# Kernel optimization log

Hardware: AMD Instinct MI355X
Metric: run time of the kernel (lower is better)

The kernel has to match this reference:

```python
import jax, jax.numpy as jnp
import numpy as np

T, B, V, D, H = 128, 64, 100000, 300, 256


def setup_inputs() -> dict:
    key = jax.random.key(0)
    ks = jax.random.split(key, 11)
    s1 = jax.random.randint(ks[0], (T, B), 0, V)
    s2 = jax.random.randint(ks[1], (T, B), 0, V)
    emb = jax.random.normal(ks[2], (V, D), jnp.float32)
    # PyTorch-style init: ih ~ N(0,0.2)/sqrt(H*D), hh ~ N(0,0.2)/sqrt(H)
    W_ih = jax.random.normal(ks[3], (4 * H, D), jnp.float32) * 0.2 / np.sqrt(H * D)
    W_hh = jax.random.normal(ks[4], (4 * H, H), jnp.float32) * 0.2 / np.sqrt(H)
    b_ih = jax.random.uniform(ks[5], (4 * H,), jnp.float32, -0.5, 0.5)
    b_ih = b_ih.at[H:2 * H].set(2.5)  # forget-gate bias boost as in source
    b_hh = jax.random.uniform(ks[6], (4 * H,), jnp.float32, -0.5, 0.5)
    b_hh = b_hh.at[H:2 * H].set(2.5)
    h0a = jax.random.normal(ks[7], (B, H), jnp.float32) * 0.01
    c0a = jax.random.normal(ks[8], (B, H), jnp.float32) * 0.01
    h0b = jax.random.normal(ks[9], (B, H), jnp.float32) * 0.01
    c0b = jax.random.normal(ks[10], (B, H), jnp.float32) * 0.01
    return {"s1": s1, "s2": s2, "emb": emb, "W_ih": W_ih, "W_hh": W_hh,
            "b_ih": b_ih, "b_hh": b_hh, "h0a": h0a, "c0a": c0a,
            "h0b": h0b, "c0b": c0b}


def _lstm_final_hidden(x, h0, c0, W_ih, W_hh, b_ih, b_hh):
    # x: [T, B, D]. PyTorch gate order: i, f, g, o.
    hdim = h0.shape[-1]
    # Precompute input contribution for all timesteps: [T, B, 4H]
    gx = jnp.einsum('tbd,gd->tbg', x, W_ih) + b_ih + b_hh

    def step(carry, gx_t):
        h, c = carry
        gates = gx_t + h @ W_hh.T  # [B, 4H]
        i = jax.nn.sigmoid(gates[:, 0 * hdim:1 * hdim])
        f = jax.nn.sigmoid(gates[:, 1 * hdim:2 * hdim])
        g = jnp.tanh(gates[:, 2 * hdim:3 * hdim])
        o = jax.nn.sigmoid(gates[:, 3 * hdim:4 * hdim])
        c = f * c + i * g
        h = o * jnp.tanh(c)
        return (h, c), None

    (h, _), _ = jax.lax.scan(step, (h0, c0), gx)
    return h  # [B, H]


def reference(s1, s2, emb, W_ih, W_hh, b_ih, b_hh, h0a, c0a, h0b, c0b):
    xa = emb[s1]  # [T, B, D]
    xb = emb[s2]
    ha = _lstm_final_hidden(xa, h0a, c0a, W_ih, W_hh, b_ih, b_hh)
    hb = _lstm_final_hidden(xb, h0b, c0b, W_ih, W_hh, b_ih, b_hh)
    norm = jnp.sum(jnp.abs(ha - hb), axis=1)  # L1 over hidden dim -> [B]
    y = jnp.clip(jnp.exp(-norm), 1e-7, 1.0 - 1e-7)
    return y.reshape(-1)
```

## Files before the change

kernel.cpp:

```cpp
#include <hip/hip_runtime.h>
#include <hip/hip_fp16.h>
#include <math.h>

#define TSTEPS 128

typedef _Float16 half8 __attribute__((ext_vector_type(8)));
typedef float f32x4 __attribute__((ext_vector_type(4)));
typedef __attribute__((ext_vector_type(2))) _Float16 half2v;

#if __has_builtin(__builtin_amdgcn_fdot2)
#define FDOT2(a, b, c) __builtin_amdgcn_fdot2((a), (b), (c), false)
#else
static __device__ __forceinline__ float FDOT2(half2v a, half2v b, float c) {
    return c + (float)a.x * (float)b.x + (float)a.y * (float)b.y;
}
#endif

static __device__ __forceinline__ half2v h2(unsigned u) {
    union { unsigned x; half2v h; } t; t.x = u; return t.h;
}
static __device__ __forceinline__ unsigned packh2(float lo, float hi) {
    union { unsigned x; half2v h; } t; t.h.x = (_Float16)lo; t.h.y = (_Float16)hi; return t.x;
}
static __device__ __forceinline__ float sigm(float x) { return 1.0f / (1.0f + __expf(-x)); }
static __device__ __forceinline__ float tanh_(float x) { return 1.0f - 2.0f / (1.0f + __expf(2.0f * x)); }

typedef __attribute__((address_space(1))) const unsigned GU;
typedef __attribute__((address_space(3))) unsigned LU;
static __device__ __forceinline__ void glds16(const void* g, void* l) {
    __builtin_amdgcn_global_load_lds((GU*)g, (LU*)(uintptr_t)l, 16, 0, 0);
}

__global__ __launch_bounds__(256) void prep_whh(const float* __restrict__ Whh,
                                                unsigned* __restrict__ W16T) {
    __shared__ float tile[32][259];
    const int blk = blockIdx.x, tid = threadIdx.x;
#pragma unroll
    for (int l = 0; l < 32; ++l) {
        int idx = tid + l * 256;
        int r = idx >> 8, k = idx & 255;
        tile[r][k] = Whh[(size_t)(blk * 32 + r) * 256 + k];
    }
    __syncthreads();
#pragma unroll
    for (int l = 0; l < 16; ++l) {
        int o = tid + l * 256;
        int i = o >> 5, rl = o & 31;
        W16T[(size_t)i * 1024 + blk * 32 + rl] = packh2(tile[rl][2 * i], tile[rl][2 * i + 1]);
    }
}

__global__ __launch_bounds__(256) void gather_x(
    const int* __restrict__ s1, const int* __restrict__ s2,
    const float* __restrict__ emb, _Float16* __restrict__ xf)
{
    const int G = blockIdx.x * 256 + threadIdx.x;
    const int lane = G & 63;
    const int tmp = G >> 6;
    const int ks = tmp % 10;
    const int fr = tmp / 10;
    const int m = fr * 16 + (lane & 15);
    const int tok = (m < 8192) ? s1[m] : s2[m - 8192];
    const float* row = emb + (size_t)tok * 300;
    const int k0 = ks * 32 + ((lane >> 4) & 3) * 4;
    half8 o;
#pragma unroll
    for (int c = 0; c < 2; ++c) {
        const int kc = k0 + c * 16;
#pragma unroll
        for (int j = 0; j < 4; ++j)
            o[c * 4 + j] = (_Float16)((kc + j < 300) ? row[kc + j] : 0.f);
    }
    *(half8*)(xf + (size_t)G * 8) = o;
}

__global__ __launch_bounds__(256) void gather_w(
    const float* __restrict__ Wih, _Float16* __restrict__ wf)
{
    const int G = blockIdx.x * 256 + threadIdx.x;
    const int lane = G & 63;
    const int tmp = G >> 6;
    const int ks = tmp % 10;
    const int fr = tmp / 10;
    const int n = fr * 16 + (lane & 15);
    const float* row = Wih + (size_t)n * 300;
    const int k0 = ks * 32 + ((lane >> 4) & 3) * 4;
    half8 o;
#pragma unroll
    for (int c = 0; c < 2; ++c) {
        const int kc = k0 + c * 16;
#pragma unroll
        for (int j = 0; j < 4; ++j)
            o[c * 4 + j] = (_Float16)((kc + j < 300) ? row[kc + j] : 0.f);
    }
    *(half8*)(wf + (size_t)G * 8) = o;
}

__global__ __launch_bounds__(256) void gx_gemm_mfma(
    const _Float16* __restrict__ xf, const _Float16* __restrict__ wf,
    _Float16* __restrict__ gx16)
{
    __shared__ _Float16 sm[2][8192];
    const int tid = threadIdx.x;
    const int lane = tid & 63, wv = tid >> 6;
    const int wr = wv >> 1, wc = wv & 1;
    const int bm = blockIdx.x & 127, bn = blockIdx.x >> 7;
    const int frM = bm * 8, frN = bn * 8;

    f32x4 acc[4][4] = {};

#define STAGE(buf, ks)                                                              \
    {                                                                               \
        _Pragma("unroll")                                                           \
        for (int i_ = 0; i_ < 2; ++i_) {                                            \
            const int fr_ = wv + 4 * i_;                                            \
            glds16(xf + (((size_t)(frM + fr_) * 10 + (ks)) * 64 + lane) * 8,        \
                   &sm[buf][fr_ * 512 + lane * 8]);                                 \
            glds16(wf + (((size_t)(frN + fr_) * 10 + (ks)) * 64 + lane) * 8,        \
                   &sm[buf][4096 + fr_ * 512 + lane * 8]);                          \
        }                                                                           \
    }

    STAGE(0, 0)
    for (int ks = 0; ks < 10; ++ks) {
        const int cur = ks & 1;
        if (ks < 9) {
            STAGE(cur ^ 1, ks + 1)
            asm volatile("s_waitcnt vmcnt(4)" ::: "memory");
        } else {
            asm volatile("s_waitcnt vmcnt(0)" ::: "memory");
        }
        __syncthreads();
        half8 av[4], bv[4];
#pragma unroll
        for (int i = 0; i < 4; ++i) {
            av[i] = *(const half8*)&sm[cur][(wr * 4 + i) * 512 + lane * 8];
            bv[i] = *(const half8*)&sm[cur][4096 + (wc * 4 + i) * 512 + lane * 8];
        }
#pragma unroll
        for (int i = 0; i < 4; ++i)
#pragma unroll
            for (int j = 0; j < 4; ++j)
                acc[i][j] = __builtin_amdgcn_mfma_f32_16x16x32_f16(av[i], bv[j], acc[i][j], 0, 0, 0);
        __syncthreads();
    }
#undef STAGE

    const int m0 = bm * 128 + wr * 64, n0 = bn * 128 + wc * 64;
    const int rl = ((lane >> 4) & 3) * 4, cl = lane & 15;
#pragma unroll
    for (int i = 0; i < 4; ++i)
#pragma unroll
        for (int j = 0; j < 4; ++j)
#pragma unroll
            for (int r = 0; r < 4; ++r)
                gx16[(size_t)(m0 + i * 16 + rl + r) * 1024 + n0 + j * 16 + cl] =
                    (_Float16)acc[i][j][r];
}

__global__ __launch_bounds__(512) void lstm_rec(
    const unsigned* __restrict__ W16T,
    const unsigned short* __restrict__ gx16,
    const float* __restrict__ bih, const float* __restrict__ bhh,
    const float* __restrict__ h0a, const float* __restrict__ c0a,
    const float* __restrict__ h0b, const float* __restrict__ c0b,
    float* __restrict__ hfin)
{
    extern __shared__ unsigned smem[];
    unsigned* wlds = smem;
    unsigned* hbuf = smem + 512 * 68;
    float*    pre  = (float*)(smem + 512 * 68 + 128);

    const int tid = threadIdx.x;
    const int chain = blockIdx.x;
    const int u = tid & 255, p = tid >> 8;
    const int r0 = (p << 9) + u;
    const int r1 = r0 + 256;

    const float bias0 = bih[r0] + bhh[r0];
    const float bias1 = bih[r1] + bhh[r1];

    unsigned w0[96], w1[96];
#pragma unroll
    for (int i = 0; i < 96; ++i) w0[i] = W16T[(size_t)i * 1024 + r0];
#pragma unroll
    for (int i = 0; i < 96; ++i) w1[i] = W16T[(size_t)i * 1024 + r1];
#pragma unroll
    for (int i = 0; i < 96; ++i) {
        asm volatile("" : "+v"(w0[i]));
        asm volatile("" : "+v"(w1[i]));
    }
    {
        unsigned* mb = wlds + tid * 68;
#pragma unroll
        for (int j = 0; j < 32; ++j) mb[j] = W16T[(size_t)(96 + j) * 1024 + r0];
#pragma unroll
        for (int j = 0; j < 32; ++j) mb[32 + j] = W16T[(size_t)(96 + j) * 1024 + r1];
    }

    float c_state = 0.f;
    if (p == 0) {
        const float* c0 = (chain & 64) ? c0b : c0a;
        const float* h0 = (chain & 64) ? h0b : h0a;
        c_state = c0[(chain & 63) * 256 + u];
        ((_Float16*)hbuf)[u] = (_Float16)h0[(chain & 63) * 256 + u];
    }
    __syncthreads();

    const unsigned short* gxb = gx16 + ((size_t)(chain >> 6) * 8192 + (size_t)(chain & 63)) * 1024;
    const unsigned* mb = wlds + tid * 68;

    for (int t = 0; t < TSTEPS; ++t) {
        const unsigned short gr0 = gxb[(size_t)t * 65536 + r0];
        const unsigned short gr1 = gxb[(size_t)t * 65536 + r1];

        float acc0 = 0.f, acc1 = 0.f;
#pragma unroll
        for (int cc = 0; cc < 24; ++cc) {
            const uint4 hv = *(const uint4*)&hbuf[cc * 4];
            acc0 = FDOT2(h2(w0[cc * 4 + 0]), h2(hv.x), acc0);
            acc1 = FDOT2(h2(w1[cc * 4 + 0]), h2(hv.x), acc1);
            acc0 = FDOT2(h2(w0[cc * 4 + 1]), h2(hv.y), acc0);
            acc1 = FDOT2(h2(w1[cc * 4 + 1]), h2(hv.y), acc1);
            acc0 = FDOT2(h2(w0[cc * 4 + 2]), h2(hv.z), acc0);
            acc1 = FDOT2(h2(w1[cc * 4 + 2]), h2(hv.z), acc1);
            acc0 = FDOT2(h2(w0[cc * 4 + 3]), h2(hv.w), acc0);
            acc1 = FDOT2(h2(w1[cc * 4 + 3]), h2(hv.w), acc1);
        }
#pragma unroll
        for (int cc = 0; cc < 4; ++cc) {
            const uint4 hv0 = *(const uint4*)&hbuf[96 + cc * 8];
            const uint4 hv1 = *(const uint4*)&hbuf[96 + cc * 8 + 4];
            const uint4 wa = *(const uint4*)&mb[cc * 8];
            const uint4 wb = *(const uint4*)&mb[cc * 8 + 4];
            const uint4 wc = *(const uint4*)&mb[32 + cc * 8];
            const uint4 wd = *(const uint4*)&mb[32 + cc * 8 + 4];
            acc0 = FDOT2(h2(wa.x), h2(hv0.x), acc0);  acc1 = FDOT2(h2(wc.x), h2(hv0.x), acc1);
            acc0 = FDOT2(h2(wa.y), h2(hv0.y), acc0);  acc1 = FDOT2(h2(wc.y), h2(hv0.y), acc1);
            acc0 = FDOT2(h2(wa.z), h2(hv0.z), acc0);  acc1 = FDOT2(h2(wc.z), h2(hv0.z), acc1);
            acc0 = FDOT2(h2(wa.w), h2(hv0.w), acc0);  acc1 = FDOT2(h2(wc.w), h2(hv0.w), acc1);
            acc0 = FDOT2(h2(wb.x), h2(hv1.x), acc0);  acc1 = FDOT2(h2(wd.x), h2(hv1.x), acc1);
            acc0 = FDOT2(h2(wb.y), h2(hv1.y), acc0);  acc1 = FDOT2(h2(wd.y), h2(hv1.y), acc1);
            acc0 = FDOT2(h2(wb.z), h2(hv1.z), acc0);  acc1 = FDOT2(h2(wd.z), h2(hv1.z), acc1);
            acc0 = FDOT2(h2(wb.w), h2(hv1.w), acc0);  acc1 = FDOT2(h2(wd.w), h2(hv1.w), acc1);
        }
        acc0 += (float)*(const _Float16*)&gr0 + bias0;
        acc1 += (float)*(const _Float16*)&gr1 + bias1;

        float gi = 0.f, gf = 0.f;
        if (p) {
            pre[u] = tanh_(acc0);
            pre[256 + u] = sigm(acc1);
        } else {
            gi = sigm(acc0);
            gf = sigm(acc1);
        }
        __syncthreads();
        if (!p) {
            c_state = fmaf(gf, c_state, gi * pre[u]);
            const float h = pre[256 + u] * tanh_(c_state);
            ((_Float16*)hbuf)[u] = (_Float16)h;
            if (t == TSTEPS - 1) hfin[(size_t)chain * 256 + u] = h;
        }
        __syncthreads();
    }
}

__global__ __launch_bounds__(256) void final_norm(const float* __restrict__ hfin,
                                                  float* __restrict__ out) {
    __shared__ float ws[4];
    const int b = blockIdx.x, tid = threadIdx.x;
    float d = fabsf(hfin[(size_t)b * 256 + tid] - hfin[(size_t)(64 + b) * 256 + tid]);
#pragma unroll
    for (int off = 32; off; off >>= 1) d += __shfl_down(d, off);
    if ((tid & 63) == 0) ws[tid >> 6] = d;
    __syncthreads();
    if (tid == 0) {
        float n = ws[0] + ws[1] + ws[2] + ws[3];
        float y = expf(-n);
        y = fminf(fmaxf(y, 1e-7f), 1.0f - 1e-7f);
        out[b] = y;
    }
}

extern "C" void kernel_launch(void* const* d_in, const int* in_sizes, int n_in,
                              void* d_out, int out_size, void* d_ws, size_t ws_size,
                              hipStream_t stream) {
    const int*   s1  = (const int*)d_in[0];
    const int*   s2  = (const int*)d_in[1];
    const float* emb = (const float*)d_in[2];
    const float* Wih = (const float*)d_in[3];
    const float* Whh = (const float*)d_in[4];
    const float* bih = (const float*)d_in[5];
    const float* bhh = (const float*)d_in[6];
    const float* h0a = (const float*)d_in[7];
    const float* c0a = (const float*)d_in[8];
    const float* h0b = (const float*)d_in[9];
    const float* c0b = (const float*)d_in[10];
    float* out = (float*)d_out;

    char* ws = (char*)d_ws;
    _Float16* xf   = (_Float16*)ws;
    _Float16* wfp  = (_Float16*)(ws + 10485760);
    _Float16* gx16 = (_Float16*)(ws + (size_t)16 * 1024 * 1024);
    unsigned* W16T = (unsigned*)(ws + 50331648);
    float*    hfin = (float*)(ws + 50855936);

    prep_whh<<<32, 256, 0, stream>>>(Whh, W16T);
    gather_x<<<2560, 256, 0, stream>>>(s1, s2, emb, xf);
    gather_w<<<160, 256, 0, stream>>>(Wih, wfp);
    gx_gemm_mfma<<<1024, 256, 0, stream>>>(xf, wfp, gx16);

    const int rec_lds = (512 * 68 + 128 + 512) * 4;
    lstm_rec<<<128, 512, rec_lds, stream>>>(W16T, (const unsigned short*)gx16,
                                            bih, bhh, h0a, c0a, h0b, c0b, hfin);
    final_norm<<<64, 256, 0, stream>>>(hfin, out);
}
```

Before: 419.0 us.

## Split each LSTM chain across two blocks with flag sync and coalesce embedding gather

```diff
diff --git a/kernel.cpp b/kernel.cpp
--- a/kernel.cpp
+++ b/kernel.cpp
@@ -25,6 +25,11 @@
 static __device__ __forceinline__ float sigm(float x) { return 1.0f / (1.0f + __expf(-x)); }
 static __device__ __forceinline__ float tanh_(float x) { return 1.0f - 2.0f / (1.0f + __expf(2.0f * x)); }
 
+template <int CTRL>
+static __device__ __forceinline__ float qb(float v) {
+    return __int_as_float(__builtin_amdgcn_update_dpp(0, __float_as_int(v), CTRL, 0xF, 0xF, true));
+}
+
 typedef __attribute__((address_space(1))) const unsigned GU;
 typedef __attribute__((address_space(3))) unsigned LU;
 static __device__ __forceinline__ void glds16(const void* g, void* l) {
@@ -50,28 +55,42 @@
     }
 }
 
-__global__ __launch_bounds__(256) void gather_x(
+__global__ __launch_bounds__(256) void gather_x2(
     const int* __restrict__ s1, const int* __restrict__ s2,
     const float* __restrict__ emb, _Float16* __restrict__ xf)
 {
-    const int G = blockIdx.x * 256 + threadIdx.x;
-    const int lane = G & 63;
-    const int tmp = G >> 6;
-    const int ks = tmp % 10;
-    const int fr = tmp / 10;
-    const int m = fr * 16 + (lane & 15);
-    const int tok = (m < 8192) ? s1[m] : s2[m - 8192];
-    const float* row = emb + (size_t)tok * 300;
-    const int k0 = ks * 32 + ((lane >> 4) & 3) * 4;
-    half8 o;
-#pragma unroll
-    for (int c = 0; c < 2; ++c) {
-        const int kc = k0 + c * 16;
-#pragma unroll
-        for (int j = 0; j < 4; ++j)
-            o[c * 4 + j] = (_Float16)((kc + j < 300) ? row[kc + j] : 0.f);
-    }
-    *(half8*)(xf + (size_t)G * 8) = o;
+    __shared__ float tile[16][301];
+    __shared__ int toks[16];
+    const int fr = blockIdx.x;
+    const int tid = threadIdx.x;
+    if (tid < 16) {
+        const int m = fr * 16 + tid;
+        toks[tid] = (m < 8192) ? s1[m] : s2[m - 8192];
+    }
+    __syncthreads();
+#pragma unroll
+    for (int l = 0; l < 19; ++l) {
+        const int flat = tid + l * 256;
+        if (flat < 4800) {
+            const int row = flat / 300, k = flat - row * 300;
+            tile[row][k] = emb[(size_t)toks[row] * 300 + k];
+        }
+    }
+    __syncthreads();
+    unsigned* outp = (unsigned*)xf + (size_t)fr * 2560;
+#pragma unroll
+    for (int l = 0; l < 10; ++l) {
+        const int d = tid + l * 256;
+        const int ks = d >> 8;
+        const int rem = d & 255;
+        const int lane = rem >> 2, ep = rem & 3;
+        const int e0 = 2 * ep, c = e0 >> 2, j0 = e0 & 3;
+        const int row = lane & 15;
+        const int k = ks * 32 + (lane >> 4) * 4 + c * 16 + j0;
+        const float f0 = (k < 300) ? tile[row][k] : 0.f;
+        const float f1 = (k + 1 < 300) ? tile[row][k + 1] : 0.f;
+        outp[d] = packh2(f0, f1);
+    }
 }
 
 __global__ __launch_bounds__(256) void gather_w(
@@ -158,111 +177,123 @@
                     (_Float16)acc[i][j][r];
 }
 
-__global__ __launch_bounds__(512) void lstm_rec(
+__global__ __launch_bounds__(512, 2) void lstm_rec2(
     const unsigned* __restrict__ W16T,
     const unsigned short* __restrict__ gx16,
     const float* __restrict__ bih, const float* __restrict__ bhh,
     const float* __restrict__ h0a, const float* __restrict__ c0a,
     const float* __restrict__ h0b, const float* __restrict__ c0b,
+    unsigned* __restrict__ hx,
+    unsigned* __restrict__ flags,
     float* __restrict__ hfin)
 {
     extern __shared__ unsigned smem[];
-    unsigned* wlds = smem;
-    unsigned* hbuf = smem + 512 * 68;
-    float*    pre  = (float*)(smem + 512 * 68 + 128);
+    _Float16* hbuf = (_Float16*)smem;
 
     const int tid = threadIdx.x;
-    const int chain = blockIdx.x;
-    const int u = tid & 255, p = tid >> 8;
-    const int r0 = (p << 9) + u;
-    const int r1 = r0 + 256;
-
-    const float bias0 = bih[r0] + bhh[r0];
-    const float bias1 = bih[r1] + bhh[r1];
-
-    unsigned w0[96], w1[96];
-#pragma unroll
-    for (int i = 0; i < 96; ++i) w0[i] = W16T[(size_t)i * 1024 + r0];
-#pragma unroll
-    for (int i = 0; i < 96; ++i) w1[i] = W16T[(size_t)i * 1024 + r1];
-#pragma unroll
-    for (int i = 0; i < 96; ++i) {
-        asm volatile("" : "+v"(w0[i]));
-        asm volatile("" : "+v"(w1[i]));
-    }
-    {
-        unsigned* mb = wlds + tid * 68;
-#pragma unroll
-        for (int j = 0; j < 32; ++j) mb[j] = W16T[(size_t)(96 + j) * 1024 + r0];
-#pragma unroll
-        for (int j = 0; j < 32; ++j) mb[32 + j] = W16T[(size_t)(96 + j) * 1024 + r1];
-    }
-
-    float c_state = 0.f;
-    if (p == 0) {
-        const float* c0 = (chain & 64) ? c0b : c0a;
-        const float* h0 = (chain & 64) ? h0b : h0a;
-        c_state = c0[(chain & 63) * 256 + u];
-        ((_Float16*)hbuf)[u] = (_Float16)h0[(chain & 63) * 256 + u];
-    }
-    __syncthreads();
-
-    const unsigned short* gxb = gx16 + ((size_t)(chain >> 6) * 8192 + (size_t)(chain & 63)) * 1024;
-    const unsigned* mb = wlds + tid * 68;
+    const int chain = blockIdx.x & 127;
+    const int hf = blockIdx.x >> 7;
+    const int u = tid >> 2;
+    const int q = tid & 3;
+    const int unit = hf * 128 + u;
+    const int r = q * 256 + unit;
+
+    unsigned wo[64], wp[64];
+    const int ob = hf * 64, pb = (1 - hf) * 64;
+#pragma unroll
+    for (int i = 0; i < 64; ++i) wo[i] = W16T[(size_t)(ob + i) * 1024 + r];
+#pragma unroll
+    for (int i = 0; i < 64; ++i) wp[i] = W16T[(size_t)(pb + i) * 1024 + r];
+#pragma unroll
+    for (int i = 0; i < 64; ++i) {
+        asm volatile("" : "+v"(wo[i]));
+        asm volatile("" : "+v"(wp[i]));
+    }
+
+    const float bias = bih[r] + bhh[r];
+    const int seq = chain >> 6, b = chain & 63;
+    const float* h0 = seq ? h0b : h0a;
+    const float* c0 = seq ? c0b : c0a;
+    float c = c0[b * 256 + unit];
+    const float h0v = h0[b * 256 + unit];
+
+    if (q == 0) {
+        hbuf[u] = (_Float16)h0v;
+        union { _Float16 f; unsigned short s; } cv; cv.f = (_Float16)h0v;
+        ((unsigned short*)(hx + (((size_t)chain * 2 + 0) * 2 + hf) * 64))[u] = cv.s;
+    }
+    asm volatile("s_waitcnt vmcnt(0)" ::: "memory");
+    __syncthreads();
+    if (tid == 0) {
+        __hip_atomic_store(&flags[chain * 2 + hf], 1u, __ATOMIC_RELEASE, __HIP_MEMORY_SCOPE_AGENT);
+        while (__hip_atomic_load(&flags[chain * 2 + (1 - hf)], __ATOMIC_ACQUIRE,
+                                 __HIP_MEMORY_SCOPE_AGENT) < 1u) {}
+    }
+    __syncthreads();
+
+    const unsigned short* gxr = gx16 + ((size_t)seq * 8192 + b) * 1024 + r;
 
     for (int t = 0; t < TSTEPS; ++t) {
-        const unsigned short gr0 = gxb[(size_t)t * 65536 + r0];
-        const unsigned short gr1 = gxb[(size_t)t * 65536 + r1];
-
-        float acc0 = 0.f, acc1 = 0.f;
-#pragma unroll
-        for (int cc = 0; cc < 24; ++cc) {
-            const uint4 hv = *(const uint4*)&hbuf[cc * 4];
-            acc0 = FDOT2(h2(w0[cc * 4 + 0]), h2(hv.x), acc0);
-            acc1 = FDOT2(h2(w1[cc * 4 + 0]), h2(hv.x), acc1);
-            acc0 = FDOT2(h2(w0[cc * 4 + 1]), h2(hv.y), acc0);
-            acc1 = FDOT2(h2(w1[cc * 4 + 1]), h2(hv.y), acc1);
-            acc0 = FDOT2(h2(w0[cc * 4 + 2]), h2(hv.z), acc0);
-            acc1 = FDOT2(h2(w1[cc * 4 + 2]), h2(hv.z), acc1);
-            acc0 = FDOT2(h2(w0[cc * 4 + 3]), h2(hv.w), acc0);
-            acc1 = FDOT2(h2(w1[cc * 4 + 3]), h2(hv.w), acc1);
-        }
-#pragma unroll
-        for (int cc = 0; cc < 4; ++cc) {
-            const uint4 hv0 = *(const uint4*)&hbuf[96 + cc * 8];
-            const uint4 hv1 = *(const uint4*)&hbuf[96 + cc * 8 + 4];
-            const uint4 wa = *(const uint4*)&mb[cc * 8];
-            const uint4 wb = *(const uint4*)&mb[cc * 8 + 4];
-            const uint4 wc = *(const uint4*)&mb[32 + cc * 8];
-            const uint4 wd = *(const uint4*)&mb[32 + cc * 8 + 4];
-            acc0 = FDOT2(h2(wa.x), h2(hv0.x), acc0);  acc1 = FDOT2(h2(wc.x), h2(hv0.x), acc1);
-            acc0 = FDOT2(h2(wa.y), h2(hv0.y), acc0);  acc1 = FDOT2(h2(wc.y), h2(hv0.y), acc1);
-            acc0 = FDOT2(h2(wa.z), h2(hv0.z), acc0);  acc1 = FDOT2(h2(wc.z), h2(hv0.z), acc1);
-            acc0 = FDOT2(h2(wa.w), h2(hv0.w), acc0);  acc1 = FDOT2(h2(wc.w), h2(hv0.w), acc1);
-            acc0 = FDOT2(h2(wb.x), h2(hv1.x), acc0);  acc1 = FDOT2(h2(wd.x), h2(hv1.x), acc1);
-            acc0 = FDOT2(h2(wb.y), h2(hv1.y), acc0);  acc1 = FDOT2(h2(wd.y), h2(hv1.y), acc1);
-            acc0 = FDOT2(h2(wb.z), h2(hv1.z), acc0);  acc1 = FDOT2(h2(wd.z), h2(hv1.z), acc1);
-            acc0 = FDOT2(h2(wb.w), h2(hv1.w), acc0);  acc1 = FDOT2(h2(wd.w), h2(hv1.w), acc1);
-        }
-        acc0 += (float)*(const _Float16*)&gr0 + bias0;
-        acc1 += (float)*(const _Float16*)&gr1 + bias1;
-
-        float gi = 0.f, gf = 0.f;
-        if (p) {
-            pre[u] = tanh_(acc0);
-            pre[256 + u] = sigm(acc1);
-        } else {
-            gi = sigm(acc0);
-            gf = sigm(acc1);
-        }
-        __syncthreads();
-        if (!p) {
-            c_state = fmaf(gf, c_state, gi * pre[u]);
-            const float h = pre[256 + u] * tanh_(c_state);
-            ((_Float16*)hbuf)[u] = (_Float16)h;
-            if (t == TSTEPS - 1) hfin[(size_t)chain * 256 + u] = h;
-        }
-        __syncthreads();
+        const unsigned short gbits = gxr[(size_t)t * 65536];
+        const int buf = t & 1;
+
+        const uint4* php = (const uint4*)(hx + (((size_t)chain * 2 + buf) * 2 + (1 - hf)) * 64);
+        uint4 ph[16];
+#pragma unroll
+        for (int j = 0; j < 16; ++j) ph[j] = php[j];
+
+        const uint4* hop = (const uint4*)(smem + buf * 64);
+        float a0 = 0.f, a1 = 0.f, a2 = 0.f, a3 = 0.f;
+#pragma unroll
+        for (int j = 0; j < 16; ++j) {
+            const uint4 hv = hop[j];
+            a0 = FDOT2(h2(wo[4 * j + 0]), h2(hv.x), a0);
+            a1 = FDOT2(h2(wo[4 * j + 1]), h2(hv.y), a1);
+            a2 = FDOT2(h2(wo[4 * j + 2]), h2(hv.z), a2);
+            a3 = FDOT2(h2(wo[4 * j + 3]), h2(hv.w), a3);
+        }
+#pragma unroll
+        for (int j = 0; j < 16; ++j) {
+            a0 = FDOT2(h2(wp[4 * j + 0]), h2(ph[j].x), a0);
+            a1 = FDOT2(h2(wp[4 * j + 1]), h2(ph[j].y), a1);
+            a2 = FDOT2(h2(wp[4 * j + 2]), h2(ph[j].z), a2);
+            a3 = FDOT2(h2(wp[4 * j + 3]), h2(ph[j].w), a3);
+        }
+        const float pre = ((a0 + a1) + (a2 + a3)) + (float)*(const _Float16*)&gbits + bias;
+
+        const bool isg = (q == 2);
+        const float xs = isg ? 2.f * pre : pre;
+        const float ev = __expf(-xs);
+        const float vv = 1.f / (1.f + ev);
+        const float act = isg ? 2.f * vv - 1.f : vv;
+
+        const float gi = qb<0x00>(act);
+        const float gf = qb<0x55>(act);
+        const float gg = qb<0xAA>(act);
+        const float go = qb<0xFF>(act);
+        c = fmaf(gf, c, gi * gg);
+        const float h = go * tanh_(c);
+
+        if (q == 0) {
+            hbuf[(buf ^ 1) * 128 + u] = (_Float16)h;
+            if (t < TSTEPS - 1) {
+                union { _Float16 f; unsigned short s; } cv; cv.f = (_Float16)h;
+                ((unsigned short*)(hx + (((size_t)chain * 2 + (buf ^ 1)) * 2 + hf) * 64))[u] = cv.s;
+            } else {
+                hfin[(size_t)chain * 256 + unit] = h;
+            }
+        }
+        if (t < TSTEPS - 1) {
+            asm volatile("s_waitcnt vmcnt(0)" ::: "memory");
+            __syncthreads();
+            if (tid == 0) {
+                __hip_atomic_store(&flags[chain * 2 + hf], (unsigned)(t + 2),
+                                   __ATOMIC_RELEASE, __HIP_MEMORY_SCOPE_AGENT);
+                while (__hip_atomic_load(&flags[chain * 2 + (1 - hf)], __ATOMIC_ACQUIRE,
+                                         __HIP_MEMORY_SCOPE_AGENT) < (unsigned)(t + 2)) {}
+            }
+            __syncthreads();
+        }
     }
 }
 
@@ -300,19 +331,23 @@
     float* out = (float*)d_out;
 
     char* ws = (char*)d_ws;
-    _Float16* xf   = (_Float16*)ws;
-    _Float16* wfp  = (_Float16*)(ws + 10485760);
-    _Float16* gx16 = (_Float16*)(ws + (size_t)16 * 1024 * 1024);
-    unsigned* W16T = (unsigned*)(ws + 50331648);
-    float*    hfin = (float*)(ws + 50855936);
+    _Float16* xf    = (_Float16*)ws;
+    _Float16* wfp   = (_Float16*)(ws + 10485760);
+    _Float16* gx16  = (_Float16*)(ws + (size_t)16 * 1024 * 1024);
+    unsigned* W16T  = (unsigned*)(ws + 50331648);
+    float*    hfin  = (float*)(ws + 50855936);
+    unsigned* hx    = (unsigned*)(ws + 50987008);
+    unsigned* flags = (unsigned*)(ws + 51118080);
+
+    hipMemsetAsync(flags, 0, 4096, stream);
 
     prep_whh<<<32, 256, 0, stream>>>(Whh, W16T);
-    gather_x<<<2560, 256, 0, stream>>>(s1, s2, emb, xf);
+    gather_x2<<<1024, 256, 0, stream>>>(s1, s2, emb, xf);
     gather_w<<<160, 256, 0, stream>>>(Wih, wfp);
     gx_gemm_mfma<<<1024, 256, 0, stream>>>(xf, wfp, gx16);
 
-    const int rec_lds = (512 * 68 + 128 + 512) * 4;
-    lstm_rec<<<128, 512, rec_lds, stream>>>(W16T, (const unsigned short*)gx16,
-                                            bih, bhh, h0a, c0a, h0b, c0b, hfin);
+    lstm_rec2<<<256, 512, 90112, stream>>>(W16T, (const unsigned short*)gx16,
+                                           bih, bhh, h0a, c0a, h0b, c0b,
+                                           hx, flags, hfin);
     final_norm<<<64, 256, 0, stream>>>(hfin, out);
 }
```

New measurement: 1.026 ms. +144.9%, slower.
